# Optimization experiments

Hardware: AMD Instinct MI355X
Metric: run time of the kernel (lower is better)

Reference implementation:

```python
import itertools
import jax, jax.numpy as jnp
import numpy as np
from jax import lax

B, C, F, V, D = 128, 8, 16, 2048, 512
SPL = 1  # spl_resolution


def _crn(objs, cond, Ws, bs, gWs, gbs, rng):
    """CRN with max_subset_size == num_objects (so start_scale = 1).
    objs: [N, n, D] or [B, n, T, D] (object axis = 1); cond broadcasts over g.
    Ws/bs: stacked [n-1, D, 2D]/[n-1, D]; gWs/gbs optional gating bank.
    Returns list of n-2 outputs (scales n-1 .. 2)."""
    n = objs.shape[1]
    outs = []
    for scaleID in range(1, n - 1):
        scale = n - scaleID  # scales = [n, n-1, ..., 2]
        rels = list(itertools.combinations(range(n), scale))
        spl = min(SPL, len(rels))
        idxs = rng.choice(len(rels), spl, replace=False)
        acc = 0.0
        for idx in idxs:
            sel = np.asarray(rels[int(idx)])
            g = objs[:, sel].mean(axis=1)  # gather subset, mean over objects
            h = jnp.concatenate([g, jnp.broadcast_to(cond, g.shape)], axis=-1)
            z = jax.nn.elu(h @ Ws[scaleID].T + bs[scaleID])
            if gWs is not None:
                z = z * jax.nn.sigmoid(h @ gWs[scaleID].T + gbs[scaleID])
            acc = acc + z
        outs.append(acc / spl)
    return outs


def _lstm_last_h(x, W_ih, W_hh, b_ih, b_hh):
    """torch.nn.LSTM (batch_first, 1 layer, unidirectional): return h_n [B, D]."""
    Bx, Dh = x.shape[0], W_hh.shape[1]

    def step(carry, xt):
        h, c = carry
        gates = xt @ W_ih.T + b_ih + h @ W_hh.T + b_hh
        i, f, g, o = jnp.split(gates, 4, axis=-1)
        c = jax.nn.sigmoid(f) * c + jax.nn.sigmoid(i) * jnp.tanh(g)
        h = jax.nn.sigmoid(o) * jnp.tanh(c)
        return (h, c), None

    h0 = jnp.zeros((Bx, Dh), x.dtype)
    (h, _), _ = lax.scan(step, (h0, h0), jnp.swapaxes(x, 0, 1))
    return h


def setup_inputs():
    key = jax.random.key(0)
    ks = iter(jax.random.split(key, 48))

    def nrm(shape, scale=0.02):
        return jax.random.normal(next(ks), shape, jnp.float32) * scale

    return {
        "appearance_video_feat": jax.random.normal(next(ks), (B, C, F, V), jnp.float32),
        "motion_video_feat": jax.random.normal(next(ks), (B, C, V), jnp.float32),
        "question_embedding": jax.random.normal(next(ks), (B, D), jnp.float32),
        "Wq": nrm((D, D)), "bq": jnp.zeros((D,), jnp.float32),
        "Wm": nrm((D, V)), "bm": jnp.zeros((D,), jnp.float32),
        "Wa": nrm((D, V)), "ba": jnp.zeros((D,), jnp.float32),
        "Wvm": nrm((D, D)), "bvm": jnp.zeros((D,), jnp.float32),
        "W_ih": nrm((4 * D, V)), "W_hh": nrm((4 * D, D)),
        "b_ih": jnp.zeros((4 * D,), jnp.float32), "b_hh": jnp.zeros((4 * D,), jnp.float32),
        "W1": nrm((F - 1, D, 2 * D)), "b1": jnp.zeros((F - 1, D), jnp.float32),
        "W2": nrm((F - 3, D, 2 * D)), "b2": jnp.zeros((F - 3, D), jnp.float32),
        "gW2": nrm((F - 3, D, 2 * D)), "gb2": jnp.zeros((F - 3, D), jnp.float32),
        "W3": nrm((C - 1, D, 2 * D)), "b3": jnp.zeros((C - 1, D), jnp.float32),
        "W4": nrm((C - 3, D, 2 * D)), "b4": jnp.zeros((C - 3, D), jnp.float32),
        "gW4": nrm((C - 3, D, 2 * D)), "gb4": jnp.zeros((C - 3, D), jnp.float32),
    }


def reference(appearance_video_feat, motion_video_feat, question_embedding,
              Wq, bq, Wm, bm, Wa, ba, Wvm, bvm, W_ih, W_hh, b_ih, b_hh,
              W1, b1, W2, b2, gW2, gb2, W3, b3, W4, b4, gW4, gb4):
    rng = np.random.RandomState(0)  # deterministic subset sampling (trace-time)
    q_proj = question_embedding @ Wq.T + bq  # [B, D]

    # ---- clip level, vectorized over (batch, clip) ----
    app_proj = jnp.einsum('bcfv,dv->bcfd', appearance_video_feat, Wa) + ba
    mot_proj = motion_video_feat @ Wm.T + bm  # [B, C, D]
    objs = app_proj.reshape(B * C, F, D)
    cond_m = mot_proj.reshape(B * C, D)
    crn_m = _crn(objs, cond_m, W1, b1, None, None, rng)
    objs2 = jnp.stack(crn_m, axis=1)                           # [B*C, F-2, D]
    cond_q = jnp.broadcast_to(q_proj[:, None, :], (B, C, D)).reshape(B * C, D)
    crn_q = _crn(objs2, cond_q, W2, b2, gW2, gb2, rng)
    clip_out = jnp.stack(crn_q, axis=1).reshape(B, C, F - 4, D)

    # ---- video level ----
    h_n = _lstm_last_h(motion_video_feat, W_ih, W_hh, b_ih, b_hh)  # [B, D]
    vm_proj = (h_n @ Wvm.T + bvm)[:, None, :]                      # [B, 1, D]
    crn_vm = _crn(clip_out, vm_proj, W3, b3, None, None, rng)
    objs4 = jnp.stack(crn_vm, axis=1)                              # [B, C-2, F-4, D]
    crn_vq = _crn(objs4, q_proj[:, None, :], W4, b4, gW4, gb4, rng)
    out = jnp.stack(crn_vq, axis=1).reshape(B, (C - 4) * (F - 4), D)
    return out
```

## Files before the change

### kernel.cpp

```cpp
#include <hip/hip_runtime.h>
#include <vector>
#include <cstdint>
#include <cstddef>


typedef unsigned short u16;
typedef unsigned int u32;

typedef _Float16 h16;
typedef h16  h8 __attribute__((ext_vector_type(8)));
typedef h16  h4 __attribute__((ext_vector_type(4)));
typedef float f4 __attribute__((ext_vector_type(4)));
typedef float f32x4 __attribute__((ext_vector_type(4)));

enum { EPI_NONE=0, EPI_ELU=1, EPI_GATE=2 };

__device__ __forceinline__ h8 ld16f_as_h8(const float* p){
  f4 x0 = *(const f4*)p, x1 = *(const f4*)(p+4);
  h4 a = __builtin_convertvector(x0, h4);
  h4 b = __builtin_convertvector(x1, h4);
  return __builtin_shufflevector(a, b, 0,1,2,3,4,5,6,7);
}

__device__ __forceinline__ void stage_f32(const float* rowbase, long ld, int k0,
                                          h16* lds, int tid){
  const int r = tid >> 1, half = tid & 1;
  const float* src = rowbase + (long)r*ld + k0 + half*16;
  h8 g0 = ld16f_as_h8(src);
  h8 g1 = ld16f_as_h8(src + 8);
  const int s = (r>>1)&3;
  const int kq0 = half*2;
  *(h8*)&lds[r*32 + ((kq0      ^ s)<<3)] = g0;
  *(h8*)&lds[r*32 + (((kq0+1) ^ s)<<3)] = g1;
}

__device__ __forceinline__ void stage_async(const h16* base, long ld, int k0,
                                            h16* lds, int wave, int lane){
#pragma unroll
  for(int cc=0;cc<2;cc++){
    const int c = wave*2+cc;
    const int r = c*16 + (lane>>2);
    const int kq = (lane&3) ^ ((r>>1)&3);
    const h16* g = base + (long)r*ld + k0 + kq*8;
    __builtin_amdgcn_global_load_lds(
        (const __attribute__((address_space(1))) void*)g,
        (__attribute__((address_space(3))) void*)&lds[c*512], 16, 0, 0);
  }
}

template<typename AT, typename OutT, int EPI>
__global__ __launch_bounds__(256) void gemm_k(
    const AT* __restrict__ A, long sA, int lda,
    const h16* __restrict__ W, long sW,
    const float* __restrict__ bias1, long sB1,
    const float* __restrict__ bias2,
    OutT* __restrict__ out, long sOut,
    int K, int rdiv, long stride_b, long stride_t)
{
  __shared__ __align__(16) h16 As[128*32];
  __shared__ __align__(16) h16 Bs[128*32];
  const int tid  = threadIdx.x;
  const int lane = tid & 63;
  const int wave = tid >> 6;
  const int z = blockIdx.z;
  const int row0 = blockIdx.x*128;
  const int col0 = blockIdx.y*128;
  const AT*  Ab = A + (long)z*sA + (long)row0*lda;
  const h16* Wb = W + (long)z*sW + (long)col0*K;

  f32x4 acc[4][4];
#pragma unroll
  for(int i=0;i<4;i++)
#pragma unroll
    for(int j=0;j<4;j++)
#pragma unroll
      for(int e=0;e<4;e++) acc[i][j][e]=0.f;

  const int wm = wave >> 1, wn = wave & 1;
  const int lrow = lane & 15, quad = lane >> 4;

  for(int k0=0;k0<K;k0+=32){
    if constexpr (sizeof(AT)==4) stage_f32((const float*)Ab, lda, k0, As, tid);
    else                         stage_async((const h16*)Ab, lda, k0, As, wave, lane);
    stage_async(Wb, K, k0, Bs, wave, lane);
    __syncthreads();
    h8 af[4], bfr[4];
#pragma unroll
    for(int i=0;i<4;i++){
      const int ra = wm*64 + i*16 + lrow;
      af[i]  = *(const h8*)&As[ra*32 + ((quad ^ ((ra>>1)&3))<<3)];
      const int rb = wn*64 + i*16 + lrow;
      bfr[i] = *(const h8*)&Bs[rb*32 + ((quad ^ ((rb>>1)&3))<<3)];
    }
#pragma unroll
    for(int i=0;i<4;i++)
#pragma unroll
      for(int j=0;j<4;j++)
        acc[i][j] = __builtin_amdgcn_mfma_f32_16x16x32_f16(af[i], bfr[j], acc[i][j], 0,0,0);
    __syncthreads();
  }

  const float* b1 = bias1 ? bias1 + (long)z*sB1 : nullptr;
  OutT* ob = out + (long)z*sOut;
  float bv[4]; int gcv[4];
#pragma unroll
  for(int j=0;j<4;j++){
    const int gc = col0 + wn*64 + j*16 + lrow;
    gcv[j]=gc;
    float b = b1 ? b1[gc] : 0.f;
    if(bias2) b += bias2[gc];
    bv[j]=b;
  }
#pragma unroll
  for(int i=0;i<4;i++){
#pragma unroll
    for(int e=0;e<4;e++){
      const int gr = row0 + wm*64 + i*16 + quad*4 + e;
      const long rowbase = (long)(gr/rdiv)*stride_b + (long)(gr%rdiv)*stride_t;
#pragma unroll
      for(int j=0;j<4;j++){
        float v = acc[i][j][e] + bv[j];
        const long idx = rowbase + gcv[j];
        if constexpr (EPI==EPI_NONE){
          ob[idx] = (OutT)v;
        } else if constexpr (EPI==EPI_ELU){
          v = v>0.f ? v : expm1f(v);
          ob[idx] = (OutT)v;
        } else {
          const float g = 1.f/(1.f+expf(-v));
          const float prev = (float)ob[idx];
          ob[idx] = (OutT)(prev*g);
        }
      }
    }
  }
}

struct CvtArgs { const float* src[8]; h16* dst[8]; int blk0[9]; };

__global__ __launch_bounds__(256) void cvt_k(CvtArgs a){
  int b = blockIdx.x, t = 0;
  while(b >= a.blk0[t+1]) t++;
  const float* s = a.src[t];
  h16* d = a.dst[t];
  const long base = (long)(b - a.blk0[t])*8192 + threadIdx.x*8;
#pragma unroll
  for(int i=0;i<4;i++){
    const long off = base + (long)i*2048;
    *(h8*)(d+off) = ld16f_as_h8(s+off);
  }
}

struct BuildArgs {
  const h16* src; const h16* cond; h16* H;
  long strideH;
  int rdiv; long stride_hi, stride_lo, obj_stride;
  int cdiv;
  int nsel[16];
  int sel[16][16];
};

__global__ __launch_bounds__(256) void build_h_k(BuildArgs p){
  const int s = blockIdx.z;
  const int tid = threadIdx.x;
  const int r  = blockIdx.x*2 + (tid>>7);
  const int d0 = (tid&127)*8;
  h16* Hp = p.H + (long)s*p.strideH + (long)r*1024 + d0;
  if(d0 < 512){
    const long base = (long)(r/p.rdiv)*p.stride_hi + (long)(r%p.rdiv)*p.stride_lo + d0;
    const int cnt = p.nsel[s];
    float f[8];
#pragma unroll
    for(int e=0;e<8;e++) f[e]=0.f;
    for(int i=0;i<cnt;i++){
      union { h16 h[8]; uint4 q; } v;
      v.q = *(const uint4*)(p.src + base + (long)p.sel[s][i]*p.obj_stride);
#pragma unroll
      for(int e=0;e<8;e++) f[e] += (float)v.h[e];
    }
    const float inv = 1.f/(float)cnt;
    union { h16 h[8]; uint4 q; } o;
#pragma unroll
    for(int e=0;e<8;e++) o.h[e]=(h16)(f[e]*inv);
    *(uint4*)Hp = o.q;
  } else {
    const long cidx = (long)(r/p.cdiv)*512 + (d0-512);
    *(uint4*)Hp = *(const uint4*)(p.cond + cidx);
  }
}

__global__ __launch_bounds__(256) void lstm_cell_k(
  const h16* __restrict__ xb, const h16* __restrict__ hW,
  float* __restrict__ c, h16* __restrict__ hout, int t)
{
  const int idx = blockIdx.x*256 + threadIdx.x;
  const int b = idx >> 9, d = idx & 511;
  const h16* xr = xb + (long)(b*8 + t)*2048;
  float gi = (float)xr[d], gf = (float)xr[512+d], gg = (float)xr[1024+d], go = (float)xr[1536+d];
  if(hW){
    const h16* hr = hW + (long)b*2048;
    gi += (float)hr[d]; gf += (float)hr[512+d]; gg += (float)hr[1024+d]; go += (float)hr[1536+d];
  }
  const float cp = (t==0)?0.f:c[idx];
  const float si = 1.f/(1.f+expf(-gi));
  const float sf = 1.f/(1.f+expf(-gf));
  const float so = 1.f/(1.f+expf(-go));
  const float cn = sf*cp + si*tanhf(gg);
  const float hn = so*tanhf(cn);
  c[idx]=cn; hout[idx]=(h16)hn;
}

namespace {

struct MT19937 {
  u32 mt[624]; int mti;
  void seed(u32 s){
    mt[0]=s;
    for(int i=1;i<624;i++) mt[i]=1812433253u*(mt[i-1]^(mt[i-1]>>30))+(u32)i;
    mti=624;
  }
  u32 next(){
    if(mti>=624){
      for(int i=0;i<624;i++){
        u32 y=(mt[i]&0x80000000u)|(mt[(i+1)%624]&0x7fffffffu);
        mt[i]=mt[(i+397)%624]^(y>>1)^((y&1u)?2567483615u:0u);
      }
      mti=0;
    }
    u32 y=mt[mti++];
    y^=y>>11; y^=(y<<7)&2636928640u; y^=(y<<15)&4022730752u; y^=y>>18;
    return y;
  }
};

static unsigned long long rand_interval(MT19937& r, unsigned long long mx){
  if(!mx) return 0;
  unsigned long long mask=mx;
  mask|=mask>>1; mask|=mask>>2; mask|=mask>>4; mask|=mask>>8; mask|=mask>>16; mask|=mask>>32;
  unsigned long long v;
  do { v = (unsigned long long)r.next() & mask; } while (v > mx);
  return v;
}

static long choice_one(MT19937& r, long N){
  std::vector<int> a((size_t)N);
  for(long i=0;i<N;i++) a[(size_t)i]=(int)i;
  for(long i=N-1;i>=1;i--){
    long j=(long)rand_interval(r,(unsigned long long)i);
    int t=a[(size_t)i]; a[(size_t)i]=a[(size_t)j]; a[(size_t)j]=t;
  }
  return a[0];
}

struct SelSet { int cnt; int idx[16]; };

static void compute_sels(SelSet* l1, SelSet* l2, SelSet* l3, SelSet* l4){
  long long Bn[20][20] = {};
  for(int i=0;i<20;i++){ Bn[i][0]=1; for(int j=1;j<=i;j++) Bn[i][j]=Bn[i-1][j-1]+Bn[i-1][j]; }
  MT19937 rng; rng.seed(0);
  auto dolevel=[&](int n, int nsc, SelSet* outs){
    for(int s=0;s<nsc;s++){
      const int scale = n-1-s;
      const long long N = Bn[n][scale];
      long long rem = (long long)choice_one(rng,(long)N);
      int x=0;
      for(int pos=0;pos<scale;pos++){
        for(int v=x;;v++){
          const long long c = Bn[n-1-v][scale-1-pos];
          if(rem < c){ outs[s].idx[pos]=v; x=v+1; break; }
          rem -= c;
        }
      }
      outs[s].cnt=scale;
    }
  };
  dolevel(16,14,l1);
  dolevel(14,12,l2);
  dolevel(8, 6, l3);
  dolevel(6, 4, l4);
}

}

extern "C" void kernel_launch(void* const* d_in, const int* in_sizes, int n_in,
                              void* d_out, int out_size, void* d_ws, size_t ws_size,
                              hipStream_t stream) {
  (void)in_sizes; (void)n_in; (void)out_size; (void)ws_size;

  const float* app  = (const float*)d_in[0];
  const float* mot  = (const float*)d_in[1];
  const float* ques = (const float*)d_in[2];
  const float* Wq =(const float*)d_in[3];  const float* bq =(const float*)d_in[4];
  const float* Wm =(const float*)d_in[5];  const float* bm =(const float*)d_in[6];
  const float* Wa =(const float*)d_in[7];  const float* ba =(const float*)d_in[8];
  const float* Wvm=(const float*)d_in[9];  const float* bvm=(const float*)d_in[10];
  const float* Wih=(const float*)d_in[11]; const float* Whh=(const float*)d_in[12];
  const float* bih=(const float*)d_in[13]; const float* bhh=(const float*)d_in[14];
  const float* W1 =(const float*)d_in[15]; const float* b1 =(const float*)d_in[16];
  const float* W2 =(const float*)d_in[17]; const float* b2 =(const float*)d_in[18];
  const float* gW2=(const float*)d_in[19]; const float* gb2=(const float*)d_in[20];
  const float* W3 =(const float*)d_in[21]; const float* b3 =(const float*)d_in[22];
  const float* W4 =(const float*)d_in[23]; const float* b4 =(const float*)d_in[24];
  const float* gW4=(const float*)d_in[25]; const float* gb4=(const float*)d_in[26];

  char* wsp = (char*)d_ws;
  h16* app_proj = (h16*)(wsp + 0);
  h16* crnm     = (h16*)(wsp + 16777216);
  h16* crnq     = (h16*)(wsp + 31457280);
  h16* crnvm    = (h16*)(wsp + 44040192);
  h16* Hbuf     = (h16*)(wsp + 53477376);
  char* Warena  =        wsp + 66060288;
  h16* mot_proj = (h16*)(wsp + 91226112);
  h16* q_proj   = (h16*)(wsp + 92274688);
  h16* vm_proj  = (h16*)(wsp + 92405760);

  h16*  xb16 = (h16*)((char*)crnm + 0);
  h16*  hWb  = (h16*)((char*)crnm + 4194304);
  float* cbuf= (float*)((char*)crnm + 4718592);
  h16*  h0   = (h16*)((char*)crnm + 4980736);
  h16*  h1   = (h16*)((char*)crnm + 5111808);

  h16* Wa16  = (h16*)(Warena + 0);
  h16* Wm16  = (h16*)(Warena + 2097152);
  h16* Wq16  = (h16*)(Warena + 4194304);
  h16* Wvm16 = (h16*)(Warena + 4718592);
  h16* Wih16 = (h16*)(Warena + 5242880);
  h16* Whh16 = (h16*)(Warena + 13631488);
  h16* mot16 = (h16*)(Warena + 15728640);
  h16* ques16= (h16*)(Warena + 19922944);
  h16* W1_16 = (h16*)(Warena + 0);
  h16* W2_16 = (h16*)(Warena + 0);
  h16* gW2_16= (h16*)(Warena + 12582912);
  h16* W3_16 = (h16*)(Warena + 0);
  h16* W4_16 = (h16*)(Warena + 6291456);
  h16* gW4_16= (h16*)(Warena + 10485760);

  float* outp = (float*)d_out;

  SelSet s1[14], s2[12], s3[6], s4[4];
  compute_sels(s1,s2,s3,s4);

  auto cvt = [&](std::initializer_list<const float*> srcs,
                 std::initializer_list<h16*> dsts,
                 std::initializer_list<long> ns){
    CvtArgs a{}; int t=0, blk=0; a.blk0[0]=0;
    auto si=srcs.begin(); auto di=dsts.begin(); auto ni=ns.begin();
    for(; si!=srcs.end(); ++si,++di,++ni,++t){
      a.src[t]=*si; a.dst[t]=*di; blk += (int)(*ni/8192); a.blk0[t+1]=blk;
    }
    for(int i=t+1;i<=8;i++) a.blk0[i]=blk;
    cvt_k<<<dim3(blk),256,0,stream>>>(a);
  };

  cvt({Wa, Wm, Wq, Wvm, Wih, Whh, mot, ques},
      {Wa16, Wm16, Wq16, Wvm16, Wih16, Whh16, mot16, ques16},
      {1048576, 1048576, 262144, 262144, 4194304, 1048576, 2097152, 65536});

  gemm_k<float,h16,EPI_NONE><<<dim3(128,4,1),256,0,stream>>>(
      app,0,2048, Wa16,0, ba,0, nullptr, app_proj,0, 2048, 16384,0,512);
  gemm_k<h16,h16,EPI_NONE><<<dim3(8,4,1),256,0,stream>>>(
      mot16,0,2048, Wm16,0, bm,0, nullptr, mot_proj,0, 2048, 1024,0,512);
  gemm_k<h16,h16,EPI_NONE><<<dim3(1,4,1),256,0,stream>>>(
      ques16,0,512, Wq16,0, bq,0, nullptr, q_proj,0, 512, 128,0,512);
  gemm_k<h16,h16,EPI_NONE><<<dim3(8,16,1),256,0,stream>>>(
      mot16,0,2048, Wih16,0, bih,0, bhh, xb16,0, 2048, 1024,0,2048);

  h16* hping[2] = {h0, h1};
  lstm_cell_k<<<dim3(256),256,0,stream>>>(xb16, nullptr, cbuf, hping[0], 0);
  for(int t=1;t<8;t++){
    gemm_k<h16,h16,EPI_NONE><<<dim3(1,16,1),256,0,stream>>>(
        hping[(t-1)&1],0,512, Whh16,0, nullptr,0, nullptr,
        hWb,0, 512, 128,0,2048);
    lstm_cell_k<<<dim3(256),256,0,stream>>>(xb16, hWb, cbuf, hping[t&1], t);
  }
  gemm_k<h16,h16,EPI_NONE><<<dim3(1,4,1),256,0,stream>>>(
      hping[1],0,512, Wvm16,0, bvm,0, nullptr, vm_proj,0, 512, 128,0,512);

  auto fill_chunk=[&](BuildArgs& a, const SelSet* ss, int z0, int nz){
    for(int s=0;s<nz;s++){ a.nsel[s]=ss[z0+s].cnt;
      for(int i=0;i<ss[z0+s].cnt;i++) a.sel[s][i]=ss[z0+s].idx[i]; }
  };

  cvt({W1+524288},{W1_16},{7340032});
  {
    const int z0s[3]={0,6,12}, nzs[3]={6,6,2};
    for(int ch=0;ch<3;ch++){
      const int z0=z0s[ch], nz=nzs[ch];
      BuildArgs a = {}; a.src=app_proj; a.cond=mot_proj; a.H=Hbuf;
      a.strideH=1048576; a.rdiv=1024; a.stride_hi=0; a.stride_lo=8192;
      a.obj_stride=512; a.cdiv=1; fill_chunk(a,s1,z0,nz);
      build_h_k<<<dim3(512,1,nz),256,0,stream>>>(a);
      gemm_k<h16,h16,EPI_ELU><<<dim3(8,4,nz),256,0,stream>>>(
          Hbuf,1048576,1024, W1_16+(long)z0*524288,524288,
          b1+(long)(z0+1)*512,512, nullptr,
          crnm+(long)z0*524288,524288, 1024, 1024,0,512);
    }
  }
  cvt({W2+524288, gW2+524288},{W2_16, gW2_16},{6291456, 6291456});
  {
    const int z0s[2]={0,6}, nzs[2]={6,6};
    for(int ch=0;ch<2;ch++){
      const int z0=z0s[ch], nz=nzs[ch];
      BuildArgs a = {}; a.src=crnm; a.cond=q_proj; a.H=Hbuf;
      a.strideH=1048576; a.rdiv=1024; a.stride_hi=0; a.stride_lo=512;
      a.obj_stride=524288; a.cdiv=8; fill_chunk(a,s2,z0,nz);
      build_h_k<<<dim3(512,1,nz),256,0,stream>>>(a);
      gemm_k<h16,h16,EPI_ELU><<<dim3(8,4,nz),256,0,stream>>>(
          Hbuf,1048576,1024, W2_16+(long)z0*524288,524288,
          b2+(long)(z0+1)*512,512, nullptr,
          crnq+(long)z0*524288,524288, 1024, 1024,0,512);
      gemm_k<h16,h16,EPI_GATE><<<dim3(8,4,nz),256,0,stream>>>(
          Hbuf,1048576,1024, gW2_16+(long)z0*524288,524288,
          gb2+(long)(z0+1)*512,512, nullptr,
          crnq+(long)z0*524288,524288, 1024, 1024,0,512);
    }
  }
  cvt({W3+524288, W4+524288, gW4+524288},{W3_16, W4_16, gW4_16},
      {3145728, 2097152, 2097152});
  {
    const int z0s[2]={0,4}, nzs[2]={4,2};
    for(int ch=0;ch<2;ch++){
      const int z0=z0s[ch], nz=nzs[ch];
      BuildArgs a = {}; a.src=crnq; a.cond=vm_proj; a.H=Hbuf;
      a.strideH=1572864; a.rdiv=12; a.stride_hi=4096; a.stride_lo=524288;
      a.obj_stride=512; a.cdiv=12; fill_chunk(a,s3,z0,nz);
      build_h_k<<<dim3(768,1,nz),256,0,stream>>>(a);
      gemm_k<h16,h16,EPI_ELU><<<dim3(12,4,nz),256,0,stream>>>(
          Hbuf,1572864,1024, W3_16+(long)z0*524288,524288,
          b3+(long)(z0+1)*512,512, nullptr,
          crnvm+(long)z0*786432,786432, 1024, 1536,0,512);
    }
  }
  {
    BuildArgs a = {}; a.src=crnvm; a.cond=q_proj; a.H=Hbuf;
    a.strideH=1572864; a.rdiv=1536; a.stride_hi=0; a.stride_lo=512;
    a.obj_stride=786432; a.cdiv=12; fill_chunk(a,s4,0,4);
    build_h_k<<<dim3(768,1,4),256,0,stream>>>(a);
    gemm_k<h16,float,EPI_ELU><<<dim3(12,4,4),256,0,stream>>>(
        Hbuf,1572864,1024, W4_16,524288, b4+512,512, nullptr,
        outp,6144, 1024, 12,24576,512);
    gemm_k<h16,float,EPI_GATE><<<dim3(12,4,4),256,0,stream>>>(
        Hbuf,1572864,1024, gW4_16,524288, gb4+512,512, nullptr,
        outp,6144, 1024, 12,24576,512);
  }
}
```

Baseline: 1.032 ms.

## Double-buffer GEMM LDS tiles and load fp32 A asynchronously into LDS

The GEMM main loop now keeps two LDS buffers, so the next K-tile is fetched while MFMAs run on the current one. Explicit vmcnt waits and raw barriers replace __syncthreads. The fp32 A operand is now copied straight to LDS with global_load_lds, using a swizzled layout, and converted to fp16 when fragments are read, instead of being converted in registers before the LDS store. The cost is double the LDS footprint (more for fp32 A), which may lower occupancy, and hand-written waitcnt counts that must match the number of issued loads.

Result: faster. 959.3 us (-7.0%).

```diff
diff --git a/kernel.cpp b/kernel.cpp
--- a/kernel.cpp
+++ b/kernel.cpp
@@ -20,18 +20,6 @@
   h4 a = __builtin_convertvector(x0, h4);
   h4 b = __builtin_convertvector(x1, h4);
   return __builtin_shufflevector(a, b, 0,1,2,3,4,5,6,7);
-}
-
-__device__ __forceinline__ void stage_f32(const float* rowbase, long ld, int k0,
-                                          h16* lds, int tid){
-  const int r = tid >> 1, half = tid & 1;
-  const float* src = rowbase + (long)r*ld + k0 + half*16;
-  h8 g0 = ld16f_as_h8(src);
-  h8 g1 = ld16f_as_h8(src + 8);
-  const int s = (r>>1)&3;
-  const int kq0 = half*2;
-  *(h8*)&lds[r*32 + ((kq0      ^ s)<<3)] = g0;
-  *(h8*)&lds[r*32 + (((kq0+1) ^ s)<<3)] = g1;
 }
 
 __device__ __forceinline__ void stage_async(const h16* base, long ld, int k0,
@@ -45,6 +33,20 @@
     __builtin_amdgcn_global_load_lds(
         (const __attribute__((address_space(1))) void*)g,
         (__attribute__((address_space(3))) void*)&lds[c*512], 16, 0, 0);
+  }
+}
+
+__device__ __forceinline__ void stage_f32_lds(const float* base, long ld, int k0,
+                                              float* lds, int wave, int lane){
+#pragma unroll
+  for(int cc=0;cc<4;cc++){
+    const int c = wave*4+cc;
+    const int r = c*8 + (lane>>3);
+    const int g = (lane&7) ^ ((lane>>3)&7);
+    const float* gp = base + (long)r*ld + k0 + g*4;
+    __builtin_amdgcn_global_load_lds(
+        (const __attribute__((address_space(1))) void*)gp,
+        (__attribute__((address_space(3))) void*)&lds[c*256], 16, 0, 0);
   }
 }
 
@@ -57,8 +59,10 @@
     OutT* __restrict__ out, long sOut,
     int K, int rdiv, long stride_b, long stride_t)
 {
-  __shared__ __align__(16) h16 As[128*32];
-  __shared__ __align__(16) h16 Bs[128*32];
+  constexpr bool AF32 = (sizeof(AT)==4);
+  constexpr int ABYTES = AF32 ? 16384 : 8192;
+  __shared__ __align__(16) char AsR[2][ABYTES];
+  __shared__ __align__(16) h16 Bs[2][128*32];
   const int tid  = threadIdx.x;
   const int lane = tid & 63;
   const int wave = tid >> 6;
@@ -78,26 +82,59 @@
 
   const int wm = wave >> 1, wn = wave & 1;
   const int lrow = lane & 15, quad = lane >> 4;
-
-  for(int k0=0;k0<K;k0+=32){
-    if constexpr (sizeof(AT)==4) stage_f32((const float*)Ab, lda, k0, As, tid);
-    else                         stage_async((const h16*)Ab, lda, k0, As, wave, lane);
-    stage_async(Wb, K, k0, Bs, wave, lane);
-    __syncthreads();
+  const int nt = K >> 5;
+
+  auto stage = [&](int buf, int k0){
+    if constexpr (AF32) stage_f32_lds((const float*)Ab, lda, k0, (float*)AsR[buf], wave, lane);
+    else                stage_async((const h16*)Ab, lda, k0, (h16*)AsR[buf], wave, lane);
+    stage_async(Wb, K, k0, &Bs[buf][0], wave, lane);
+  };
+
+  stage(0, 0);
+  for(int t=0;t<nt;t++){
+    const int cur = t&1;
+    if(t+1 < nt){
+      stage(cur^1, (t+1)<<5);
+      if constexpr (AF32) asm volatile("s_waitcnt vmcnt(6)" ::: "memory");
+      else                asm volatile("s_waitcnt vmcnt(4)" ::: "memory");
+    } else {
+      asm volatile("s_waitcnt vmcnt(0)" ::: "memory");
+    }
+    __builtin_amdgcn_s_barrier();
+
     h8 af[4], bfr[4];
+    if constexpr (AF32){
+      const float* As32 = (const float*)AsR[cur];
+#pragma unroll
+      for(int i=0;i<4;i++){
+        const int ra = wm*64 + i*16 + lrow;
+        const int s = ra & 7;
+        const float* pr = As32 + ra*32;
+        f4 x0 = *(const f4*)(pr + ((((quad<<1)   ) ^ s)<<2));
+        f4 x1 = *(const f4*)(pr + ((((quad<<1)|1 ) ^ s)<<2));
+        h4 a0 = __builtin_convertvector(x0, h4);
+        h4 a1 = __builtin_convertvector(x1, h4);
+        af[i] = __builtin_shufflevector(a0, a1, 0,1,2,3,4,5,6,7);
+      }
+    } else {
+      const h16* As = (const h16*)AsR[cur];
+#pragma unroll
+      for(int i=0;i<4;i++){
+        const int ra = wm*64 + i*16 + lrow;
+        af[i] = *(const h8*)&As[ra*32 + ((quad ^ ((ra>>1)&3))<<3)];
+      }
+    }
 #pragma unroll
     for(int i=0;i<4;i++){
-      const int ra = wm*64 + i*16 + lrow;
-      af[i]  = *(const h8*)&As[ra*32 + ((quad ^ ((ra>>1)&3))<<3)];
       const int rb = wn*64 + i*16 + lrow;
-      bfr[i] = *(const h8*)&Bs[rb*32 + ((quad ^ ((rb>>1)&3))<<3)];
+      bfr[i] = *(const h8*)&Bs[cur][rb*32 + ((quad ^ ((rb>>1)&3))<<3)];
     }
 #pragma unroll
     for(int i=0;i<4;i++)
 #pragma unroll
       for(int j=0;j<4;j++)
         acc[i][j] = __builtin_amdgcn_mfma_f32_16x16x32_f16(af[i], bfr[j], acc[i][j], 0,0,0);
-    __syncthreads();
+    __builtin_amdgcn_s_barrier();
   }
 
   const float* b1 = bias1 ? bias1 + (long)z*sB1 : nullptr;
```

## Double-buffer LDS tiles in GEMM to overlap global loads with MFMA

Applied to the files above, without the earlier changes.

Switches the GEMM main loop to two LDS buffers for A and W. While MFMAs run on the current tile, the next tile is prefetched: async global-to-LDS for the fp16 operands, and register loads for the fp32 A operand that are converted and committed after compute. This hides global memory latency and removes one barrier per k-step. In exchange it doubles LDS use (32KB per block), which may lower occupancy, and the prefetched fp32 values add register pressure.

Measured after the change: 977.6 us. 1.06x faster.

```diff
diff --git a/kernel.cpp b/kernel.cpp
--- a/kernel.cpp
+++ b/kernel.cpp
@@ -20,18 +20,6 @@
   h4 a = __builtin_convertvector(x0, h4);
   h4 b = __builtin_convertvector(x1, h4);
   return __builtin_shufflevector(a, b, 0,1,2,3,4,5,6,7);
-}
-
-__device__ __forceinline__ void stage_f32(const float* rowbase, long ld, int k0,
-                                          h16* lds, int tid){
-  const int r = tid >> 1, half = tid & 1;
-  const float* src = rowbase + (long)r*ld + k0 + half*16;
-  h8 g0 = ld16f_as_h8(src);
-  h8 g1 = ld16f_as_h8(src + 8);
-  const int s = (r>>1)&3;
-  const int kq0 = half*2;
-  *(h8*)&lds[r*32 + ((kq0      ^ s)<<3)] = g0;
-  *(h8*)&lds[r*32 + (((kq0+1) ^ s)<<3)] = g1;
 }
 
 __device__ __forceinline__ void stage_async(const h16* base, long ld, int k0,
@@ -46,6 +34,30 @@
         (const __attribute__((address_space(1))) void*)g,
         (__attribute__((address_space(3))) void*)&lds[c*512], 16, 0, 0);
   }
+}
+
+__device__ __forceinline__ void a_load(const float* Ab, long lda, int k0,
+                                       int tid, f4* x){
+  const int r = tid >> 1, half = tid & 1;
+  const float* src = Ab + (long)r*lda + k0 + half*16;
+  x[0] = *(const f4*)src;
+  x[1] = *(const f4*)(src+4);
+  x[2] = *(const f4*)(src+8);
+  x[3] = *(const f4*)(src+12);
+}
+
+__device__ __forceinline__ void a_commit(const f4* x, h16* lds, int tid){
+  const int r = tid >> 1, half = tid & 1;
+  h4 a0 = __builtin_convertvector(x[0], h4);
+  h4 a1 = __builtin_convertvector(x[1], h4);
+  h4 a2 = __builtin_convertvector(x[2], h4);
+  h4 a3 = __builtin_convertvector(x[3], h4);
+  h8 g0 = __builtin_shufflevector(a0, a1, 0,1,2,3,4,5,6,7);
+  h8 g1 = __builtin_shufflevector(a2, a3, 0,1,2,3,4,5,6,7);
+  const int s = (r>>1)&3;
+  const int kq0 = half*2;
+  *(h8*)&lds[r*32 + ((kq0      ^ s)<<3)] = g0;
+  *(h8*)&lds[r*32 + (((kq0+1) ^ s)<<3)] = g1;
 }
 
 template<typename AT, typename OutT, int EPI>
@@ -57,8 +69,9 @@
     OutT* __restrict__ out, long sOut,
     int K, int rdiv, long stride_b, long stride_t)
 {
-  __shared__ __align__(16) h16 As[128*32];
-  __shared__ __align__(16) h16 Bs[128*32];
+  constexpr bool AF32 = (sizeof(AT)==4);
+  __shared__ __align__(16) h16 As[2][128*32];
+  __shared__ __align__(16) h16 Bs[2][128*32];
   const int tid  = threadIdx.x;
   const int lane = tid & 63;
   const int wave = tid >> 6;
@@ -78,25 +91,44 @@
 
   const int wm = wave >> 1, wn = wave & 1;
   const int lrow = lane & 15, quad = lane >> 4;
-
-  for(int k0=0;k0<K;k0+=32){
-    if constexpr (sizeof(AT)==4) stage_f32((const float*)Ab, lda, k0, As, tid);
-    else                         stage_async((const h16*)Ab, lda, k0, As, wave, lane);
-    stage_async(Wb, K, k0, Bs, wave, lane);
-    __syncthreads();
+  const int nt = K >> 5;
+
+  f4 ar[4];
+  if constexpr (AF32){
+    a_load((const float*)Ab, lda, 0, tid, ar);
+    a_commit(ar, &As[0][0], tid);
+  } else {
+    stage_async((const h16*)Ab, lda, 0, &As[0][0], wave, lane);
+  }
+  stage_async(Wb, K, 0, &Bs[0][0], wave, lane);
+  __syncthreads();
+
+  for(int t=0;t<nt;t++){
+    const int cur = t&1, nxt = cur^1;
+    const bool pf = (t+1 < nt);
+    if(pf){
+      const int k1 = (t+1)<<5;
+      if constexpr (AF32) a_load((const float*)Ab, lda, k1, tid, ar);
+      else                stage_async((const h16*)Ab, lda, k1, &As[nxt][0], wave, lane);
+      stage_async(Wb, K, k1, &Bs[nxt][0], wave, lane);
+    }
+
     h8 af[4], bfr[4];
 #pragma unroll
     for(int i=0;i<4;i++){
       const int ra = wm*64 + i*16 + lrow;
-      af[i]  = *(const h8*)&As[ra*32 + ((quad ^ ((ra>>1)&3))<<3)];
+      af[i]  = *(const h8*)&As[cur][ra*32 + ((quad ^ ((ra>>1)&3))<<3)];
       const int rb = wn*64 + i*16 + lrow;
-      bfr[i] = *(const h8*)&Bs[rb*32 + ((quad ^ ((rb>>1)&3))<<3)];
+      bfr[i] = *(const h8*)&Bs[cur][rb*32 + ((quad ^ ((rb>>1)&3))<<3)];
     }
 #pragma unroll
     for(int i=0;i<4;i++)
 #pragma unroll
       for(int j=0;j<4;j++)
         acc[i][j] = __builtin_amdgcn_mfma_f32_16x16x32_f16(af[i], bfr[j], acc[i][j], 0,0,0);
+
+    if constexpr (AF32){ if(pf) a_commit(ar, &As[nxt][0], tid); }
+
     __syncthreads();
   }
 
```
